# Kernel optimization log

Measured on AMD Instinct MI355X. Metric: run time of the kernel, lower is better.

## Reference

```python
import jax, jax.numpy as jnp
import numpy as np

B, D, K, L, C = 1024, 512, 255, 256, 80  # batch, feat, internal nodes, leaves, classes
DEPTH = 8  # complete binary tree: 2^8 = 256 leaves


def _build_res_path():
    # res_path[l, k] = 1 if internal node k is on leaf l's path and leaf goes left,
    # -1 if it goes right, 0 if node k not on the path (matches build_tree_squeeze).
    rp = np.zeros((L, K), dtype=np.int32)
    for leaf in range(L):
        node = 0
        for d in range(DEPTH):
            bit = (leaf >> (DEPTH - 1 - d)) & 1  # 0 -> left, 1 -> right
            rp[leaf, node] = 1 if bit == 0 else -1
            node = 2 * node + 1 + bit
    return jnp.asarray(rp)


def setup_inputs() -> dict:
    key = jax.random.key(0)
    k1, k2, k3, k4 = jax.random.split(key, 4)
    x = jax.random.normal(k1, (B, D), dtype=jnp.float32)
    node_embeddings = jax.random.normal(k2, (K, D), dtype=jnp.float32)
    leaf_W = jax.random.normal(k3, (L * C, D), dtype=jnp.float32) * (1.0 / np.sqrt(D))
    leaf_b = jax.random.normal(k4, (L * C,), dtype=jnp.float32) * 0.01
    res_path = _build_res_path()
    return {"x": x, "node_embeddings": node_embeddings, "leaf_W": leaf_W,
            "leaf_b": leaf_b, "res_path": res_path}


def reference(x, node_embeddings, leaf_W, leaf_b, res_path):
    # L2-normalize node embeddings, cosine-sim routing probabilities
    ne = node_embeddings / jnp.linalg.norm(node_embeddings, axis=-1, keepdims=True)
    node_sim = jax.nn.sigmoid(jnp.einsum('bc,kc->bk', x, ne))  # [B, K]
    # leaf decision logits: Linear(D, L*C) reshaped to [B, L, C]
    leaf_dec = (jnp.einsum('bc,oc->bo', x, leaf_W) + leaf_b).reshape(x.shape[0], L, C)
    left_mask = (res_path == 1)[None]    # [1, L, K]
    right_mask = (res_path == -1)[None]  # [1, L, K]
    ns = node_sim[:, None, :]            # [B, 1, K]
    prob_left = jnp.prod(jnp.where(left_mask, ns, 1.0), axis=-1)        # [B, L]
    prob_right = jnp.prod(jnp.where(right_mask, 1.0 - ns, 1.0), axis=-1)  # [B, L]
    probs = (prob_left * prob_right)[..., None] * leaf_dec  # [B, L, C]
    return probs.sum(axis=1), node_sim
```

## Files before the change

kernel.cpp:

```cpp
#include <hip/hip_runtime.h>
#include <stdint.h>

#define B_  1024
#define D_  512
#define K_  255
#define L_  256
#define C_  80

typedef __attribute__((ext_vector_type(8))) short bf16x8;
typedef __attribute__((ext_vector_type(4))) float f32x4;
typedef __attribute__((ext_vector_type(8))) short short8;

#define GLD(gsrc, ldst) \
  __builtin_amdgcn_global_load_lds((const __attribute__((address_space(1))) void*)(gsrc), \
                                   (__attribute__((address_space(3))) void*)(ldst), 16, 0, 0)

__device__ __forceinline__ short cvt_bf16(float f) {
    unsigned u = __float_as_uint(f);
    u += 0x7FFFu + ((u >> 16) & 1u);
    return (short)(u >> 16);
}

__global__ __launch_bounds__(256) void convert_kernel(const float* __restrict__ w,
                                                      const float* __restrict__ x,
                                                      const float* __restrict__ ne,
                                                      short* __restrict__ wb,
                                                      short* __restrict__ xb,
                                                      short* __restrict__ neb) {
    __shared__ float red[256];
    const int tid = threadIdx.x;
    if (blockIdx.x < 2048) {
        size_t i0 = (size_t)blockIdx.x * 256 + tid;
        const size_t stride = 2048u * 256u;
        for (size_t v = i0; v < 1310720u; v += stride) {
            float4 a = ((const float4*)w)[v * 2];
            float4 b = ((const float4*)w)[v * 2 + 1];
            short8 o;
            o[0] = cvt_bf16(a.x); o[1] = cvt_bf16(a.y); o[2] = cvt_bf16(a.z); o[3] = cvt_bf16(a.w);
            o[4] = cvt_bf16(b.x); o[5] = cvt_bf16(b.y); o[6] = cvt_bf16(b.z); o[7] = cvt_bf16(b.w);
            ((short8*)wb)[v] = o;
        }
        for (size_t v = i0; v < 65536u; v += stride) {
            float4 a = ((const float4*)x)[v * 2];
            float4 b = ((const float4*)x)[v * 2 + 1];
            short8 o;
            o[0] = cvt_bf16(a.x); o[1] = cvt_bf16(a.y); o[2] = cvt_bf16(a.z); o[3] = cvt_bf16(a.w);
            o[4] = cvt_bf16(b.x); o[5] = cvt_bf16(b.y); o[6] = cvt_bf16(b.z); o[7] = cvt_bf16(b.w);
            ((short8*)xb)[v] = o;
        }
    } else {
        const int row = blockIdx.x - 2048;
        if (row == 255) {
            ((unsigned*)(neb + 255 * 512))[tid] = 0u;
            return;
        }
        const float2* nr = (const float2*)(ne + (size_t)row * 512);
        float2 a = nr[tid];
        red[tid] = a.x * a.x + a.y * a.y;
        __syncthreads();
        #pragma unroll
        for (int s = 128; s > 0; s >>= 1) {
            if (tid < s) red[tid] += red[tid + s];
            __syncthreads();
        }
        float inv = rsqrtf(red[0]);
        unsigned lo = (unsigned short)cvt_bf16(a.x * inv);
        unsigned hi = (unsigned short)cvt_bf16(a.y * inv);
        ((unsigned*)(neb + (size_t)row * 512))[tid] = lo | (hi << 16);
    }
}

__global__ __launch_bounds__(256) void simgemm_kernel(const short* __restrict__ xb,
                                                      const short* __restrict__ neb,
                                                      float* __restrict__ out1) {
    __shared__ __align__(16) short Ald[512 * 8];
    __shared__ __align__(16) short Bld[512 * 8];
    const int tid = threadIdx.x;
    const int lane = tid & 63, wave = tid >> 6;
    const int q = lane >> 4, r = lane & 15;
    const int mt = blockIdx.x >> 2;
    const int nt = blockIdx.x & 3;

    f32x4 acc[4];
    #pragma unroll
    for (int nf = 0; nf < 4; ++nf) acc[nf] = (f32x4){0.f, 0.f, 0.f, 0.f};

    const bf16x8* Av = (const bf16x8*)Ald;
    const bf16x8* Bv = (const bf16x8*)Bld;

    for (int kb = 0; kb < 8; ++kb) {
        __syncthreads();
        #pragma unroll
        for (int j = 0; j < 2; ++j) {
            int ph = j * 256 + tid, rr = ph >> 3, g = (ph & 7) ^ (rr & 7);
            GLD(xb + ((size_t)(mt * 64 + rr) * D_ + kb * 64 + g * 8), Ald + ph * 8);
        }
        #pragma unroll
        for (int j = 0; j < 2; ++j) {
            int ph = j * 256 + tid, cc = ph >> 3, g = (ph & 7) ^ (cc & 7);
            GLD(neb + ((size_t)(nt * 64 + cc) * D_ + kb * 64 + g * 8), Bld + ph * 8);
        }
        __syncthreads();
        #pragma unroll
        for (int ks = 0; ks < 2; ++ks) {
            const int g = ks * 4 + q;
            int rl = wave * 16 + r;
            bf16x8 af = Av[rl * 8 + (g ^ (rl & 7))];
            #pragma unroll
            for (int nf = 0; nf < 4; ++nf) {
                int cl = nf * 16 + r;
                bf16x8 bfr = Bv[cl * 8 + (g ^ (cl & 7))];
                acc[nf] = __builtin_amdgcn_mfma_f32_16x16x32_bf16(af, bfr, acc[nf], 0, 0, 0);
            }
        }
    }
    #pragma unroll
    for (int nf = 0; nf < 4; ++nf) {
        int gcol = nt * 64 + nf * 16 + r;
        if (gcol < K_) {
            #pragma unroll
            for (int i = 0; i < 4; ++i) {
                int grow = mt * 64 + wave * 16 + q * 4 + i;
                out1[(size_t)grow * K_ + gcol] = 1.f / (1.f + __expf(-acc[nf][i]));
            }
        }
    }
}

__global__ __launch_bounds__(256) void leafprob_kernel(const float* __restrict__ out1,
                                                       float* __restrict__ p_ws) {
    __shared__ float ss[K_];
    const int b = blockIdx.x, t = threadIdx.x;
    if (t < K_) ss[t] = out1[(size_t)b * K_ + t];
    __syncthreads();
    float prob = 1.f;
    int node = 0;
    #pragma unroll
    for (int d = 0; d < 8; ++d) {
        int bit = (t >> (7 - d)) & 1;
        float s = ss[node];
        prob *= bit ? (1.f - s) : s;
        node = 2 * node + 1 + bit;
    }
    p_ws[(size_t)b * L_ + t] = prob;
}

__global__ __launch_bounds__(256, 2) void gemm_kernel(const short* __restrict__ xb,
                                                      const short* __restrict__ wb,
                                                      const float* __restrict__ p,
                                                      const float* __restrict__ lb,
                                                      float* __restrict__ partial) {
    __shared__ __align__(16) short Ald[2048 * 8];
    __shared__ __align__(16) short Bld[1280 * 8];
    __shared__ float p_ld[128][4];
    __shared__ float b_ld[320];

    const int tid = threadIdx.x;
    const int lane = tid & 63, wave = tid >> 6;
    const int q = lane >> 4, r = lane & 15;
    const int wrow = wave * 32;
    const int lc = blockIdx.x & 63;
    const int mt = blockIdx.x >> 6;

    if (tid < 128) {
        #pragma unroll
        for (int li = 0; li < 4; ++li)
            p_ld[tid][li] = p[(size_t)(mt * 128 + tid) * L_ + 4 * lc + li];
    }
    {
        int c = tid;
        if (c < 320) b_ld[c] = lb[lc * 320 + c];
        if (tid < 64) b_ld[256 + tid] = lb[lc * 320 + 256 + tid];
    }

    f32x4 outacc[2][5];
    #pragma unroll
    for (int mf = 0; mf < 2; ++mf)
        #pragma unroll
        for (int nf = 0; nf < 5; ++nf)
            outacc[mf][nf] = (f32x4){0.f, 0.f, 0.f, 0.f};

    const bf16x8* Av = (const bf16x8*)Ald;
    const bf16x8* Bv = (const bf16x8*)Bld;

    for (int li = 0; li < 4; ++li) {
        const int l = lc * 4 + li;
        f32x4 dec[2][5];
        #pragma unroll
        for (int mf = 0; mf < 2; ++mf)
            #pragma unroll
            for (int nf = 0; nf < 5; ++nf)
                dec[mf][nf] = (f32x4){0.f, 0.f, 0.f, 0.f};

        for (int kb = 0; kb < 4; ++kb) {
            __syncthreads();
            #pragma unroll
            for (int j = 0; j < 8; ++j) {
                int ph = j * 256 + tid;
                int rr = ph >> 4;
                int g  = (ph & 15) ^ (rr & 15);
                GLD(xb + ((size_t)(mt * 128 + rr) * D_ + kb * 128 + g * 8), Ald + ph * 8);
            }
            #pragma unroll
            for (int j = 0; j < 5; ++j) {
                int ph = j * 256 + tid;
                int cc = ph >> 4;
                int g  = (ph & 15) ^ (cc & 15);
                GLD(wb + ((size_t)(l * C_ + cc) * D_ + kb * 128 + g * 8), Bld + ph * 8);
            }
            __syncthreads();

            #pragma unroll
            for (int ks = 0; ks < 4; ++ks) {
                const int g = ks * 4 + q;
                bf16x8 af[2], bfr[5];
                #pragma unroll
                for (int mf = 0; mf < 2; ++mf) {
                    int rl = wrow + mf * 16 + r;
                    af[mf] = Av[rl * 16 + (g ^ (rl & 15))];
                }
                #pragma unroll
                for (int nf = 0; nf < 5; ++nf) {
                    int cl = nf * 16 + r;
                    bfr[nf] = Bv[cl * 16 + (g ^ (cl & 15))];
                }
                #pragma unroll
                for (int mf = 0; mf < 2; ++mf)
                    #pragma unroll
                    for (int nf = 0; nf < 5; ++nf)
                        dec[mf][nf] = __builtin_amdgcn_mfma_f32_16x16x32_bf16(
                            af[mf], bfr[nf], dec[mf][nf], 0, 0, 0);
            }
        }

        #pragma unroll
        for (int mf = 0; mf < 2; ++mf) {
            #pragma unroll
            for (int nf = 0; nf < 5; ++nf) {
                float bv = b_ld[li * 80 + nf * 16 + r];
                #pragma unroll
                for (int i = 0; i < 4; ++i) {
                    int row = wrow + mf * 16 + q * 4 + i;
                    outacc[mf][nf][i] += p_ld[row][li] * (dec[mf][nf][i] + bv);
                }
            }
        }
    }

    const size_t rbase = (size_t)lc * B_ + mt * 128;
    #pragma unroll
    for (int mf = 0; mf < 2; ++mf)
        #pragma unroll
        for (int nf = 0; nf < 5; ++nf)
            #pragma unroll
            for (int i = 0; i < 4; ++i) {
                int row = wrow + mf * 16 + q * 4 + i;
                int col = nf * 16 + r;
                partial[(rbase + row) * C_ + col] = outacc[mf][nf][i];
            }
}

__global__ __launch_bounds__(256) void reduce_kernel(const float* __restrict__ partial,
                                                     float* __restrict__ out0) {
    int idx = blockIdx.x * 256 + threadIdx.x;
    const float4* p4 = (const float4*)partial;
    float4 s = {0.f, 0.f, 0.f, 0.f};
    #pragma unroll 8
    for (int j = 0; j < 64; ++j) {
        float4 v = p4[(size_t)j * (B_ * C_ / 4) + idx];
        s.x += v.x; s.y += v.y; s.z += v.z; s.w += v.w;
    }
    ((float4*)out0)[idx] = s;
}

extern "C" void kernel_launch(void* const* d_in, const int* in_sizes, int n_in,
                              void* d_out, int out_size, void* d_ws, size_t ws_size,
                              hipStream_t stream) {
    const float* x  = (const float*)d_in[0];
    const float* ne = (const float*)d_in[1];
    const float* lW = (const float*)d_in[2];
    const float* lb = (const float*)d_in[3];

    float* out0 = (float*)d_out;
    float* out1 = out0 + (size_t)B_ * C_;

    char* ws = (char*)d_ws;
    short* xb      = (short*)ws;
    short* neb     = (short*)(ws + (1u << 20));
    float* p_ws    = (float*)(ws + (1u << 20) + (1u << 18));
    short* wb      = (short*)(ws + (9u << 18));
    float* partial = (float*)(ws + (24u << 20));

    convert_kernel<<<2304, 256, 0, stream>>>(lW, x, ne, wb, xb, neb);
    simgemm_kernel<<<64, 256, 0, stream>>>(xb, neb, out1);
    leafprob_kernel<<<B_, 256, 0, stream>>>(out1, p_ws);
    gemm_kernel<<<512, 256, 0, stream>>>(xb, wb, p_ws, lb, partial);
    reduce_kernel<<<B_ * C_ / 1024, 256, 0, stream>>>(partial, out0);
}
```

Measured before the change: 136.5 us.

## Double-buffer LDS staging in leaf GEMM and split reduce with atomics

The leaf GEMM loop is restructured to run K in chunks of 64 with double-buffered LDS. The next leaf's weight tile, or the next x chunk, is fetched via global_load_lds while the current tile is multiplied, with one barrier per step instead of two. Routing probabilities are kept in registers and the bias term is folded in up front as sum(p*b), so the per-leaf LDS tables go away. The final reduction is split across 8x more blocks that each sum 8 partials and atomically add into an output zeroed by leafprob_kernel. This adds float-atomic nondeterminism and more barriers per K chunk.

Measured after the change: 166.4 us. 1.22x slower.

```diff
diff --git a/kernel.cpp b/kernel.cpp
--- a/kernel.cpp
+++ b/kernel.cpp
@@ -128,10 +128,12 @@
 }
 
 __global__ __launch_bounds__(256) void leafprob_kernel(const float* __restrict__ out1,
-                                                       float* __restrict__ p_ws) {
+                                                       float* __restrict__ p_ws,
+                                                       float* __restrict__ out0) {
     __shared__ float ss[K_];
     const int b = blockIdx.x, t = threadIdx.x;
     if (t < K_) ss[t] = out1[(size_t)b * K_ + t];
+    if (t < C_) out0[(size_t)b * C_ + t] = 0.f;
     __syncthreads();
     float prob = 1.f;
     int node = 0;
@@ -150,10 +152,8 @@
                                                       const float* __restrict__ p,
                                                       const float* __restrict__ lb,
                                                       float* __restrict__ partial) {
-    __shared__ __align__(16) short Ald[2048 * 8];
-    __shared__ __align__(16) short Bld[1280 * 8];
-    __shared__ float p_ld[128][4];
-    __shared__ float b_ld[320];
+    __shared__ __align__(16) short Ald[2 * 1024 * 8];
+    __shared__ __align__(16) short Bld[2 * 640 * 8];
 
     const int tid = threadIdx.x;
     const int lane = tid & 63, wave = tid >> 6;
@@ -162,88 +162,114 @@
     const int lc = blockIdx.x & 63;
     const int mt = blockIdx.x >> 6;
 
-    if (tid < 128) {
+    float pv[2][4][4];
+    #pragma unroll
+    for (int mf = 0; mf < 2; ++mf)
+        #pragma unroll
+        for (int i = 0; i < 4; ++i) {
+            int row = mt * 128 + wrow + mf * 16 + q * 4 + i;
+            float4 pw = *(const float4*)(p + (size_t)row * L_ + lc * 4);
+            pv[mf][i][0] = pw.x; pv[mf][i][1] = pw.y;
+            pv[mf][i][2] = pw.z; pv[mf][i][3] = pw.w;
+        }
+
+    f32x4 outacc[2][5];
+    #pragma unroll
+    for (int nf = 0; nf < 5; ++nf) {
+        float bv[4];
         #pragma unroll
         for (int li = 0; li < 4; ++li)
-            p_ld[tid][li] = p[(size_t)(mt * 128 + tid) * L_ + 4 * lc + li];
-    }
-    {
-        int c = tid;
-        if (c < 320) b_ld[c] = lb[lc * 320 + c];
-        if (tid < 64) b_ld[256 + tid] = lb[lc * 320 + 256 + tid];
-    }
-
-    f32x4 outacc[2][5];
-    #pragma unroll
-    for (int mf = 0; mf < 2; ++mf)
-        #pragma unroll
-        for (int nf = 0; nf < 5; ++nf)
-            outacc[mf][nf] = (f32x4){0.f, 0.f, 0.f, 0.f};
-
-    const bf16x8* Av = (const bf16x8*)Ald;
-    const bf16x8* Bv = (const bf16x8*)Bld;
-
-    for (int li = 0; li < 4; ++li) {
-        const int l = lc * 4 + li;
-        f32x4 dec[2][5];
+            bv[li] = lb[(size_t)(lc * 4 + li) * C_ + nf * 16 + r];
         #pragma unroll
         for (int mf = 0; mf < 2; ++mf)
             #pragma unroll
-            for (int nf = 0; nf < 5; ++nf)
-                dec[mf][nf] = (f32x4){0.f, 0.f, 0.f, 0.f};
-
-        for (int kb = 0; kb < 4; ++kb) {
-            __syncthreads();
-            #pragma unroll
-            for (int j = 0; j < 8; ++j) {
-                int ph = j * 256 + tid;
-                int rr = ph >> 4;
-                int g  = (ph & 15) ^ (rr & 15);
-                GLD(xb + ((size_t)(mt * 128 + rr) * D_ + kb * 128 + g * 8), Ald + ph * 8);
-            }
-            #pragma unroll
-            for (int j = 0; j < 5; ++j) {
-                int ph = j * 256 + tid;
-                int cc = ph >> 4;
-                int g  = (ph & 15) ^ (cc & 15);
-                GLD(wb + ((size_t)(l * C_ + cc) * D_ + kb * 128 + g * 8), Bld + ph * 8);
-            }
-            __syncthreads();
-
-            #pragma unroll
-            for (int ks = 0; ks < 4; ++ks) {
+            for (int i = 0; i < 4; ++i)
+                outacc[mf][nf][i] = pv[mf][i][0] * bv[0] + pv[mf][i][1] * bv[1]
+                                  + pv[mf][i][2] * bv[2] + pv[mf][i][3] * bv[3];
+    }
+
+    auto stageA = [&](int buf, int kc) {
+        #pragma unroll
+        for (int j = 0; j < 4; ++j) {
+            int ph = j * 256 + tid;
+            int rr = ph >> 3;
+            int g  = (ph & 7) ^ (rr & 7);
+            GLD(xb + ((size_t)(mt * 128 + rr)) * D_ + kc * 64 + g * 8,
+                Ald + (buf * 1024 + ph) * 8);
+        }
+    };
+    auto stageB = [&](int buf, int li, int kc) {
+        #pragma unroll
+        for (int j = 0; j < 2; ++j) {
+            int ph = j * 256 + tid;
+            int cc = ph >> 3;
+            int g  = (ph & 7) ^ (cc & 7);
+            GLD(wb + ((size_t)(lc * 4 + li) * C_ + cc) * D_ + kc * 64 + g * 8,
+                Bld + (buf * 640 + ph) * 8);
+        }
+        if (tid < 128) {
+            int ph = 512 + tid;
+            int cc = ph >> 3;
+            int g  = (ph & 7) ^ (cc & 7);
+            GLD(wb + ((size_t)(lc * 4 + li) * C_ + cc) * D_ + kc * 64 + g * 8,
+                Bld + (buf * 640 + ph) * 8);
+        }
+    };
+
+    const f32x4 z4 = {0.f, 0.f, 0.f, 0.f};
+
+    int abuf = 0, bbuf = 0;
+    stageA(0, 0);
+    stageB(0, 0, 0);
+    __syncthreads();
+
+    for (int kc = 0; kc < 8; ++kc) {
+        #pragma unroll
+        for (int li = 0; li < 4; ++li) {
+            if (li < 3) {
+                stageB(bbuf ^ 1, li + 1, kc);
+            } else if (kc < 7) {
+                stageB(bbuf ^ 1, 0, kc + 1);
+                stageA(abuf ^ 1, kc + 1);
+            }
+
+            const bf16x8* Av = (const bf16x8*)Ald + abuf * 1024;
+            const bf16x8* Bv = (const bf16x8*)Bld + bbuf * 640;
+
+            f32x4 dec[2][5];
+            #pragma unroll
+            for (int ks = 0; ks < 2; ++ks) {
                 const int g = ks * 4 + q;
                 bf16x8 af[2], bfr[5];
                 #pragma unroll
                 for (int mf = 0; mf < 2; ++mf) {
                     int rl = wrow + mf * 16 + r;
-                    af[mf] = Av[rl * 16 + (g ^ (rl & 15))];
+                    af[mf] = Av[rl * 8 + (g ^ (rl & 7))];
                 }
                 #pragma unroll
                 for (int nf = 0; nf < 5; ++nf) {
                     int cl = nf * 16 + r;
-                    bfr[nf] = Bv[cl * 16 + (g ^ (cl & 15))];
+                    bfr[nf] = Bv[cl * 8 + (g ^ (cl & 7))];
                 }
                 #pragma unroll
                 for (int mf = 0; mf < 2; ++mf)
                     #pragma unroll
                     for (int nf = 0; nf < 5; ++nf)
                         dec[mf][nf] = __builtin_amdgcn_mfma_f32_16x16x32_bf16(
-                            af[mf], bfr[nf], dec[mf][nf], 0, 0, 0);
-            }
-        }
-
-        #pragma unroll
-        for (int mf = 0; mf < 2; ++mf) {
-            #pragma unroll
-            for (int nf = 0; nf < 5; ++nf) {
-                float bv = b_ld[li * 80 + nf * 16 + r];
+                            af[mf], bfr[nf], ks == 0 ? z4 : dec[mf][nf], 0, 0, 0);
+            }
+
+            #pragma unroll
+            for (int mf = 0; mf < 2; ++mf)
                 #pragma unroll
-                for (int i = 0; i < 4; ++i) {
-                    int row = wrow + mf * 16 + q * 4 + i;
-                    outacc[mf][nf][i] += p_ld[row][li] * (dec[mf][nf][i] + bv);
-                }
-            }
+                for (int nf = 0; nf < 5; ++nf)
+                    #pragma unroll
+                    for (int i = 0; i < 4; ++i)
+                        outacc[mf][nf][i] += pv[mf][i][li] * dec[mf][nf][i];
+
+            __syncthreads();
+            bbuf ^= 1;
+            if (li == 3) abuf ^= 1;
         }
     }
 
@@ -262,15 +288,21 @@
 
 __global__ __launch_bounds__(256) void reduce_kernel(const float* __restrict__ partial,
                                                      float* __restrict__ out0) {
-    int idx = blockIdx.x * 256 + threadIdx.x;
+    const int chunk = blockIdx.x >> 3;
+    const int jg    = blockIdx.x & 7;
+    const int idx   = chunk * 256 + threadIdx.x;
     const float4* p4 = (const float4*)partial;
     float4 s = {0.f, 0.f, 0.f, 0.f};
-    #pragma unroll 8
-    for (int j = 0; j < 64; ++j) {
-        float4 v = p4[(size_t)j * (B_ * C_ / 4) + idx];
+    #pragma unroll
+    for (int j = 0; j < 8; ++j) {
+        float4 v = p4[(size_t)(jg * 8 + j) * (B_ * C_ / 4) + idx];
         s.x += v.x; s.y += v.y; s.z += v.z; s.w += v.w;
     }
-    ((float4*)out0)[idx] = s;
+    float* o = out0 + (size_t)idx * 4;
+    atomicAdd(o + 0, s.x);
+    atomicAdd(o + 1, s.y);
+    atomicAdd(o + 2, s.z);
+    atomicAdd(o + 3, s.w);
 }
 
 extern "C" void kernel_launch(void* const* d_in, const int* in_sizes, int n_in,
@@ -293,7 +325,7 @@
 
     convert_kernel<<<2304, 256, 0, stream>>>(lW, x, ne, wb, xb, neb);
     simgemm_kernel<<<64, 256, 0, stream>>>(xb, neb, out1);
-    leafprob_kernel<<<B_, 256, 0, stream>>>(out1, p_ws);
+    leafprob_kernel<<<B_, 256, 0, stream>>>(out1, p_ws, out0);
     gemm_kernel<<<512, 256, 0, stream>>>(xb, wb, p_ws, lb, partial);
-    reduce_kernel<<<B_ * C_ / 1024, 256, 0, stream>>>(partial, out0);
-}
+    reduce_kernel<<<640, 256, 0, stream>>>(partial, out0);
+}
```

## Reorder leaf GEMM loops to reuse x tile, fold bias, split reduce with atomics

Applied to the files above, without the earlier changes.

The leaf GEMM now loops K-blocks outermost and leaves innermost, so each x tile is loaded into LDS once per K-block and reused across the four leaves instead of being reloaded per leaf. Bias is folded analytically by initializing the accumulators with the p-weighted bias sum, and the per-leaf accumulation becomes a plain multiply-add with no bias term. The reduce kernel is split across eight partial groups per output chunk, using float atomics into an output that leafprob zeroes first. This raises reduce parallelism but makes the summation order nondeterministic and adds atomic traffic.

After: 140.5 us. 3.0% more time.

```diff
diff --git a/kernel.cpp b/kernel.cpp
--- a/kernel.cpp
+++ b/kernel.cpp
@@ -128,10 +128,12 @@
 }
 
 __global__ __launch_bounds__(256) void leafprob_kernel(const float* __restrict__ out1,
-                                                       float* __restrict__ p_ws) {
+                                                       float* __restrict__ p_ws,
+                                                       float* __restrict__ out0) {
     __shared__ float ss[K_];
     const int b = blockIdx.x, t = threadIdx.x;
     if (t < K_) ss[t] = out1[(size_t)b * K_ + t];
+    if (t < C_) out0[(size_t)b * C_ + t] = 0.f;
     __syncthreads();
     float prob = 1.f;
     int node = 0;
@@ -153,7 +155,6 @@
     __shared__ __align__(16) short Ald[2048 * 8];
     __shared__ __align__(16) short Bld[1280 * 8];
     __shared__ float p_ld[128][4];
-    __shared__ float b_ld[320];
 
     const int tid = threadIdx.x;
     const int lane = tid & 63, wave = tid >> 6;
@@ -163,53 +164,55 @@
     const int mt = blockIdx.x >> 6;
 
     if (tid < 128) {
+        float4 pw = *(const float4*)(p + (size_t)(mt * 128 + tid) * L_ + lc * 4);
+        p_ld[tid][0] = pw.x; p_ld[tid][1] = pw.y;
+        p_ld[tid][2] = pw.z; p_ld[tid][3] = pw.w;
+    }
+    __syncthreads();
+
+    f32x4 outacc[2][5];
+    #pragma unroll
+    for (int nf = 0; nf < 5; ++nf) {
+        float bv[4];
         #pragma unroll
         for (int li = 0; li < 4; ++li)
-            p_ld[tid][li] = p[(size_t)(mt * 128 + tid) * L_ + 4 * lc + li];
-    }
-    {
-        int c = tid;
-        if (c < 320) b_ld[c] = lb[lc * 320 + c];
-        if (tid < 64) b_ld[256 + tid] = lb[lc * 320 + 256 + tid];
-    }
-
-    f32x4 outacc[2][5];
-    #pragma unroll
-    for (int mf = 0; mf < 2; ++mf)
-        #pragma unroll
-        for (int nf = 0; nf < 5; ++nf)
-            outacc[mf][nf] = (f32x4){0.f, 0.f, 0.f, 0.f};
+            bv[li] = lb[(size_t)(lc * 4 + li) * C_ + nf * 16 + r];
+        #pragma unroll
+        for (int mf = 0; mf < 2; ++mf)
+            #pragma unroll
+            for (int i = 0; i < 4; ++i) {
+                int row = wrow + mf * 16 + q * 4 + i;
+                outacc[mf][nf][i] = p_ld[row][0] * bv[0] + p_ld[row][1] * bv[1]
+                                  + p_ld[row][2] * bv[2] + p_ld[row][3] * bv[3];
+            }
+    }
 
     const bf16x8* Av = (const bf16x8*)Ald;
     const bf16x8* Bv = (const bf16x8*)Bld;
-
-    for (int li = 0; li < 4; ++li) {
-        const int l = lc * 4 + li;
-        f32x4 dec[2][5];
-        #pragma unroll
-        for (int mf = 0; mf < 2; ++mf)
-            #pragma unroll
-            for (int nf = 0; nf < 5; ++nf)
-                dec[mf][nf] = (f32x4){0.f, 0.f, 0.f, 0.f};
-
-        for (int kb = 0; kb < 4; ++kb) {
+    const f32x4 z4 = {0.f, 0.f, 0.f, 0.f};
+
+    for (int kb = 0; kb < 4; ++kb) {
+        for (int li = 0; li < 4; ++li) {
             __syncthreads();
-            #pragma unroll
-            for (int j = 0; j < 8; ++j) {
-                int ph = j * 256 + tid;
-                int rr = ph >> 4;
-                int g  = (ph & 15) ^ (rr & 15);
-                GLD(xb + ((size_t)(mt * 128 + rr) * D_ + kb * 128 + g * 8), Ald + ph * 8);
+            if (li == 0) {
+                #pragma unroll
+                for (int j = 0; j < 8; ++j) {
+                    int ph = j * 256 + tid;
+                    int rr = ph >> 4;
+                    int g  = (ph & 15) ^ (rr & 15);
+                    GLD(xb + ((size_t)(mt * 128 + rr) * D_ + kb * 128 + g * 8), Ald + ph * 8);
+                }
             }
             #pragma unroll
             for (int j = 0; j < 5; ++j) {
                 int ph = j * 256 + tid;
                 int cc = ph >> 4;
                 int g  = (ph & 15) ^ (cc & 15);
-                GLD(wb + ((size_t)(l * C_ + cc) * D_ + kb * 128 + g * 8), Bld + ph * 8);
+                GLD(wb + ((size_t)((lc * 4 + li) * C_ + cc) * D_ + kb * 128 + g * 8), Bld + ph * 8);
             }
             __syncthreads();
 
+            f32x4 dec[2][5];
             #pragma unroll
             for (int ks = 0; ks < 4; ++ks) {
                 const int g = ks * 4 + q;
@@ -229,21 +232,18 @@
                     #pragma unroll
                     for (int nf = 0; nf < 5; ++nf)
                         dec[mf][nf] = __builtin_amdgcn_mfma_f32_16x16x32_bf16(
-                            af[mf], bfr[nf], dec[mf][nf], 0, 0, 0);
-            }
-        }
-
-        #pragma unroll
-        for (int mf = 0; mf < 2; ++mf) {
-            #pragma unroll
-            for (int nf = 0; nf < 5; ++nf) {
-                float bv = b_ld[li * 80 + nf * 16 + r];
+                            af[mf], bfr[nf], ks == 0 ? z4 : dec[mf][nf], 0, 0, 0);
+            }
+
+            #pragma unroll
+            for (int mf = 0; mf < 2; ++mf)
                 #pragma unroll
                 for (int i = 0; i < 4; ++i) {
-                    int row = wrow + mf * 16 + q * 4 + i;
-                    outacc[mf][nf][i] += p_ld[row][li] * (dec[mf][nf][i] + bv);
+                    float pf = p_ld[wrow + mf * 16 + q * 4 + i][li];
+                    #pragma unroll
+                    for (int nf = 0; nf < 5; ++nf)
+                        outacc[mf][nf][i] += pf * dec[mf][nf][i];
                 }
-            }
         }
     }
 
@@ -262,15 +262,21 @@
 
 __global__ __launch_bounds__(256) void reduce_kernel(const float* __restrict__ partial,
                                                      float* __restrict__ out0) {
-    int idx = blockIdx.x * 256 + threadIdx.x;
+    const int chunk = blockIdx.x >> 3;
+    const int jg    = blockIdx.x & 7;
+    const int idx   = chunk * 256 + threadIdx.x;
     const float4* p4 = (const float4*)partial;
     float4 s = {0.f, 0.f, 0.f, 0.f};
-    #pragma unroll 8
-    for (int j = 0; j < 64; ++j) {
-        float4 v = p4[(size_t)j * (B_ * C_ / 4) + idx];
+    #pragma unroll
+    for (int j = 0; j < 8; ++j) {
+        float4 v = p4[(size_t)(jg * 8 + j) * (B_ * C_ / 4) + idx];
         s.x += v.x; s.y += v.y; s.z += v.z; s.w += v.w;
     }
-    ((float4*)out0)[idx] = s;
+    float* o = out0 + (size_t)idx * 4;
+    atomicAdd(o + 0, s.x);
+    atomicAdd(o + 1, s.y);
+    atomicAdd(o + 2, s.z);
+    atomicAdd(o + 3, s.w);
 }
 
 extern "C" void kernel_launch(void* const* d_in, const int* in_sizes, int n_in,
@@ -293,7 +299,7 @@
 
     convert_kernel<<<2304, 256, 0, stream>>>(lW, x, ne, wb, xb, neb);
     simgemm_kernel<<<64, 256, 0, stream>>>(xb, neb, out1);
-    leafprob_kernel<<<B_, 256, 0, stream>>>(out1, p_ws);
+    leafprob_kernel<<<B_, 256, 0, stream>>>(out1, p_ws, out0);
     gemm_kernel<<<512, 256, 0, stream>>>(xb, wb, p_ws, lb, partial);
-    reduce_kernel<<<B_ * C_ / 1024, 256, 0, stream>>>(partial, out0);
-}
+    reduce_kernel<<<640, 256, 0, stream>>>(partial, out0);
+}
```
